# Optimization experiments

Hardware: AMD Instinct MI355X
Metric: run time of the kernel (lower is better)

The kernel has to match this reference:

```python
import jax, jax.numpy as jnp
import numpy as np

ALPHA = 0.5
NUM_NB = 8


def setup_inputs() -> dict:
    key = jax.random.key(0)
    k1, k2 = jax.random.split(key)
    pc1 = jax.random.normal(k1, (4, 3, 8192), dtype=jnp.float32)
    pred_flow = jax.random.normal(k2, (4, 3, 8192), dtype=jnp.float32)
    return {"pc1": pc1, "pred_flow": pred_flow}


def reference(pc1, pred_flow):
    # pc1, pred_flow: [B, 3, N] -> [B, N, 3]
    B, _, N = pc1.shape
    k = NUM_NB
    p = jnp.transpose(pc1, (0, 2, 1))         # [B, N, 3]
    f = jnp.transpose(pred_flow, (0, 2, 1))   # [B, N, 3]

    sq = jnp.sum(p * p, axis=-1)
    sqrdist = sq[:, :, None] + sq[:, None, :] - 2.0 * jnp.einsum('bnd,bmd->bnm', p, p)

    # k+1 smallest (sorted ascending), drop self (first column)
    neg_d, kidx = jax.lax.top_k(-sqrdist, k + 1)  # descending in -d == ascending in d
    dists = -neg_d[:, :, 1:]                      # [B, N, k]
    kidx = kidx[:, :, 1:]                         # [B, N, k]
    dists = jnp.maximum(dists, 0.0)

    # softmax over all N*k weights per batch
    w = jax.nn.softmax(jnp.exp(-dists / ALPHA).reshape(B, N * k), axis=1)
    w = w.reshape(B, N, k)

    # gather neighbor flows: [B, N, k, 3]
    grouped = jnp.take_along_axis(f[:, None, :, :],
                                  kidx[:, :, :, None],
                                  axis=2)
    diff = jnp.linalg.norm(grouped - f[:, :, None, :], axis=3)  # [B, N, k]
    diff_flow = (N * w * diff).sum(axis=2)                      # [B, N]
    return jnp.mean(diff_flow)
```

## Files before the change

### kernel.cpp

```cpp
#include <hip/hip_runtime.h>
#include <math.h>

#define BATCH 4
#define NQ 8192
#define KNB 8
#define K1 9
#define NB 512
#define XMIN -4.5f
#define XSCALE (NB / 9.0f)
#define CAP 21
#define THW 512
#define THS 128
#define SPART 2
#define IDXMASK 8191u
#define KEYMASK 0xFFFFE000u
#define EPS_S 1e-3f

static __device__ __forceinline__ int binOf(float x) {
  return min(max((int)((x - XMIN) * XSCALE), 0), NB - 1);
}

#define CHAIN9(KEY) { unsigned kk = (KEY); \
  _Pragma("unroll") \
  for (int j = 0; j < K1; ++j) { \
    unsigned lo = min(kk, nk[j]); unsigned hi = max(kk, nk[j]); \
    nk[j] = lo; kk = hi; } }

#define CHAIN8(KEY) { unsigned kk = (KEY); \
  _Pragma("unroll") \
  for (int j = 0; j < KNB; ++j) { \
    unsigned lo = min(kk, nk[j]); unsigned hi = max(kk, nk[j]); \
    nk[j] = lo; kk = hi; } }

#define DRAINS() { \
  for (int ii = 0; ii < cnt; ++ii) { \
    const unsigned key = sbuf[base + ii]; \
    if (key < nk[K1-1]) CHAIN9(key); \
  } \
  cnt = 0; \
  { const float td = __uint_as_float(nk[K1-1] | 0x1FFFu); \
    thetaS = fminf(thetaS, 0.5f*(td - qq) + EPS_S); } }

#define GPROC(SS, OI) { \
  if ((SS) <= thetaS) { \
    const float dd = fmaxf(fmaf(2.0f, (SS), qq), 0.0f); \
    sbuf[base + cnt] = (__float_as_uint(dd) & KEYMASK) | (OI); cnt++; } }

#define SCORE4(S0,S1,S2,S3, X,Y,Z,H) \
  float S0 = fmaf(nqx, X.x, fmaf(nqy, Y.x, fmaf(nqz, Z.x, H.x))); \
  float S1 = fmaf(nqx, X.y, fmaf(nqy, Y.y, fmaf(nqz, Z.y, H.y))); \
  float S2 = fmaf(nqx, X.z, fmaf(nqy, Y.z, fmaf(nqz, Z.z, H.z))); \
  float S3 = fmaf(nqx, X.w, fmaf(nqy, Y.w, fmaf(nqz, Z.w, H.w)));

#define BURST(CB) { \
  const int jb = (CB) << 4; \
  const int ti = (bq + jb) >> 2; \
  const float4 X0=x4[ti],X1=x4[ti+1],X2=x4[ti+2],X3=x4[ti+3]; \
  const float4 Y0=y4[ti],Y1=y4[ti+1],Y2=y4[ti+2],Y3=y4[ti+3]; \
  const float4 Z0=z4[ti],Z1=z4[ti+1],Z2=z4[ti+2],Z3=z4[ti+3]; \
  const float4 H0=h4[ti],H1=h4[ti+1],H2=h4[ti+2],H3=h4[ti+3]; \
  const uint4  I0=i4[ti],I1=i4[ti+1],I2=i4[ti+2],I3=i4[ti+3]; \
  SCORE4(s0,s1,s2,s3, X0,Y0,Z0,H0); \
  SCORE4(s4,s5,s6,s7, X1,Y1,Z1,H1); \
  SCORE4(s8,s9,sa,sb, X2,Y2,Z2,H2); \
  SCORE4(sc,sd,se,sf, X3,Y3,Z3,H3); \
  GPROC(s0,I0.x); GPROC(s1,I0.y); GPROC(s2,I0.z); GPROC(s3,I0.w); \
  GPROC(s4,I1.x); GPROC(s5,I1.y); GPROC(s6,I1.z); GPROC(s7,I1.w); \
  GPROC(s8,I2.x); GPROC(s9,I2.y); GPROC(sa,I2.z); GPROC(sb,I2.w); \
  GPROC(sc,I3.x); GPROC(sd,I3.y); GPROC(se,I3.z); GPROC(sf,I3.w); }

__global__ __launch_bounds__(256) void hist_kernel(
    const float* __restrict__ pc, unsigned* __restrict__ hist)
{
  const int t = blockIdx.x * 256 + threadIdx.x;
  const int b = t >> 13, n = t & (NQ - 1);
  atomicAdd(&hist[b * NB + binOf(pc[(size_t)b * 3 * NQ + n])], 1u);
}

__global__ __launch_bounds__(512) void prefix_kernel(
    unsigned* __restrict__ hist, unsigned* __restrict__ binStart)
{
  __shared__ unsigned sc[NB];
  const int t = threadIdx.x;
  for (int b = 0; b < BATCH; ++b) {
    const unsigned c = hist[b * NB + t];
    sc[t] = c;
    __syncthreads();
    for (int o = 1; o < NB; o <<= 1) {
      unsigned a = (t >= o) ? sc[t - o] : 0u;
      __syncthreads();
      sc[t] += a;
      __syncthreads();
    }
    const unsigned excl = sc[t] - c;
    binStart[b * (NB + 1) + t] = excl;
    hist[b * NB + t] = excl;
    if (t == NB - 1) binStart[b * (NB + 1) + NB] = NQ;
    __syncthreads();
  }
}

__global__ __launch_bounds__(256) void scatter_kernel(
    const float* __restrict__ pc, unsigned* __restrict__ cursor,
    float* __restrict__ sxs, float* __restrict__ sys, float* __restrict__ szs,
    float* __restrict__ shs, unsigned* __restrict__ ssi)
{
  const int t = blockIdx.x * 256 + threadIdx.x;
  const int b = t >> 13, n = t & (NQ - 1);
  const float* __restrict__ px = pc + (size_t)b * 3 * NQ;
  const float x = px[n], y = px[NQ + n], z = px[2 * NQ + n];
  const unsigned pos = atomicAdd(&cursor[b * NB + binOf(x)], 1u);
  const int o = b * NQ + (int)pos;
  sxs[o] = x; sys[o] = y; szs[o] = z;
  shs[o] = 0.5f * (x * x + y * y + z * z);
  ssi[o] = (unsigned)n;
}

__global__ __launch_bounds__(256) void theta_kernel(
    const float* __restrict__ sxs, const float* __restrict__ sys,
    const float* __restrict__ szs, unsigned* __restrict__ thetaOut)
{
  __shared__ float swx[THW], swy[THW], swz[THW];
  const int b = blockIdx.y, p = blockIdx.z;
  const int B0 = blockIdx.x * 256;
  const int bq = b * NQ;
  const int stg0 = min(max(B0 - 128, 0), NQ - THW);
#pragma unroll
  for (int k = 0; k < THW / 256; ++k) {
    const int i = threadIdx.x + k * 256;
    swx[i] = sxs[bq + stg0 + i];
    swy[i] = sys[bq + stg0 + i];
    swz[i] = szs[bq + stg0 + i];
  }
  __syncthreads();
  const int s = B0 + threadIdx.x;
  const float qx = swx[s - stg0], qy = swy[s - stg0], qz = swz[s - stg0];
  const int w = min(max(s - 128, stg0), stg0 + THW - 256) - stg0;
  unsigned nk[K1];
#pragma unroll
  for (int j = 0; j < K1; ++j) nk[j] = 0xFFFFFFFFu;
  for (int k = 0; k < THS; ++k) {
    const int i = w + 2 * k + p;
    const float dx = qx - swx[i], dy = qy - swy[i], dz = qz - swz[i];
    const float d = dx * dx + dy * dy + dz * dz;
    CHAIN9(__float_as_uint(d));
  }
  thetaOut[(size_t)(bq + s) * SPART + p] = nk[K1 - 1] | 0x1FFFu;
}

template<int P>
__global__ __launch_bounds__(256) void knn_kernel(
    const float* __restrict__ sxs, const float* __restrict__ sys,
    const float* __restrict__ szs, const float* __restrict__ shs,
    const unsigned* __restrict__ ssi, const unsigned* __restrict__ binStart,
    const unsigned* __restrict__ thetaIn, unsigned* __restrict__ wsK)
{
  __shared__ unsigned sbuf[256 * CAP];
  const int b = blockIdx.y, p = blockIdx.z;
  const int s = blockIdx.x * 256 + threadIdx.x;
  const int bq = b * NQ;
  const float qx = sxs[bq + s], qy = sys[bq + s], qz = szs[bq + s];
  const float nqx = -qx, nqy = -qy, nqz = -qz;
  const float qq = qx * qx + qy * qy + qz * qz;

  const uint2 th = ((const uint2*)thetaIn)[bq + s];
  const float thetaD = __uint_as_float(min(th.x, th.y));
  float thetaS = 0.5f * (thetaD - qq) + EPS_S;
  const float r = sqrtf(thetaD) * 1.0001f + 1e-7f;
  unsigned LO = binStart[b * (NB + 1) + binOf(qx - r)];
  unsigned HI = binStart[b * (NB + 1) + binOf(qx + r) + 1];
  for (int off = 32; off; off >>= 1) {
    LO = min(LO, (unsigned)__shfl_xor((int)LO, off));
    HI = max(HI, (unsigned)__shfl_xor((int)HI, off));
  }
  const int b0 = __builtin_amdgcn_readfirstlane((int)LO) >> 4;
  const int b1 = (__builtin_amdgcn_readfirstlane((int)HI) + 15) >> 4;
  const int nb = b1 - b0;
  const int st = b0 + (p * nb) / P;
  const int en = b0 + ((p + 1) * nb) / P;

  unsigned nk[K1];
#pragma unroll
  for (int j = 0; j < K1; ++j) nk[j] = 0xFFFFFFFFu;
  const unsigned base = (unsigned)threadIdx.x * CAP;
  int cnt = 0;
  const float4* __restrict__ x4 = (const float4*)sxs;
  const float4* __restrict__ y4 = (const float4*)sys;
  const float4* __restrict__ z4 = (const float4*)szs;
  const float4* __restrict__ h4 = (const float4*)shs;
  const uint4*  __restrict__ i4 = (const uint4*)ssi;

  for (int cb = st; cb < en; ++cb) {
    if (__any(cnt >= CAP - 16)) { DRAINS(); }
    BURST(cb);
  }
  DRAINS();

#pragma unroll
  for (int j = 0; j < K1; ++j)
    wsK[((size_t)(b * P + p) * K1 + j) * NQ + s] = nk[j];
}

__global__ __launch_bounds__(64) void loss_kernel(
    const float* __restrict__ pc, const float* __restrict__ pf,
    const float* __restrict__ sxs, const float* __restrict__ sys,
    const float* __restrict__ szs, const unsigned* __restrict__ ssi,
    const unsigned* __restrict__ wsK, float* __restrict__ acc,
    unsigned* __restrict__ doneCtr, float* __restrict__ out,
    int P, int nBlocks)
{
  const int b = blockIdx.y;
  const int s = blockIdx.x * 64 + threadIdx.x;
  const int bq = b * NQ;
  const float* __restrict__ px = pc + (size_t)b * 3 * NQ;
  const float* __restrict__ py = px + NQ;
  const float* __restrict__ pz = px + 2 * NQ;
  const float* __restrict__ fx = pf + (size_t)b * 3 * NQ;
  const float* __restrict__ fy = fx + NQ;
  const float* __restrict__ fz = fx + 2 * NQ;

  const unsigned qorig = ssi[bq + s];
  unsigned nk[KNB];
#pragma unroll
  for (int j = 0; j < KNB; ++j) nk[j] = 0xFFFFFFFFu;

  const int total = P * K1;
  const size_t stride0 = (size_t)b * P * K1;
  for (int m0 = 0; m0 < total; m0 += K1) {
    unsigned kb[K1];
#pragma unroll
    for (int u = 0; u < K1; ++u)
      kb[u] = wsK[(stride0 + m0 + u) * NQ + s];
#pragma unroll
    for (int u = 0; u < K1; ++u) {
      const unsigned key = kb[u];
      if ((key & IDXMASK) == qorig) continue;
      if (key < nk[KNB - 1]) CHAIN8(key);
    }
  }

  const float qx = sxs[bq + s], qy = sys[bq + s], qz = szs[bq + s];
  const float fqx = fx[qorig], fqy = fy[qorig], fqz = fz[qorig];
  float ssum = 0.f, sdsum = 0.f;
#pragma unroll
  for (int j = 0; j < KNB; ++j) {
    const int i = (int)(nk[j] & IDXMASK);
    const float dx = qx - px[i], dy = qy - py[i], dz = qz - pz[i];
    const float d = dx * dx + dy * dy + dz * dz;
    const float e = expf(expf(-2.0f * d));
    const float gx = fx[i] - fqx, gy = fy[i] - fqy, gz = fz[i] - fqz;
    const float diff = sqrtf(gx * gx + gy * gy + gz * gz);
    ssum += e; sdsum += e * diff;
  }

  for (int off = 32; off > 0; off >>= 1) {
    ssum += __shfl_down(ssum, off);
    sdsum += __shfl_down(sdsum, off);
  }
  if (threadIdx.x == 0) {
    atomicAdd(&acc[b * 2 + 0], ssum);
    atomicAdd(&acc[b * 2 + 1], sdsum);
    __threadfence();
    const unsigned done = atomicAdd(doneCtr, 1u);
    if (done == (unsigned)(nBlocks - 1)) {
      float sT = 0.f;
      for (int bb = 0; bb < BATCH; ++bb) {
        const float se = atomicAdd(&acc[bb * 2 + 0], 0.f);
        const float sd = atomicAdd(&acc[bb * 2 + 1], 0.f);
        sT += sd / se;
      }
      out[0] = sT * (1.0f / BATCH);
    }
  }
}

extern "C" void kernel_launch(void* const* d_in, const int* in_sizes, int n_in,
                              void* d_out, int out_size, void* d_ws, size_t ws_size,
                              hipStream_t stream) {
  const float* pc = (const float*)d_in[0];
  const float* pf = (const float*)d_in[1];
  float* out = (float*)d_out;

  char* w = (char*)d_ws;
  float*    acc      = (float*)w;
  unsigned* doneCtr  = (unsigned*)(w + 64);
  unsigned* hist     = (unsigned*)(w + 256);
  unsigned* binStart = (unsigned*)(w + 8448);
  const size_t SA = 16896;
  float*    sxs = (float*)(w + SA);
  float*    sys = (float*)(w + SA + 1 * 131072);
  float*    szs = (float*)(w + SA + 2 * 131072);
  float*    shs = (float*)(w + SA + 3 * 131072);
  unsigned* ssi = (unsigned*)(w + SA + 4 * 131072);
  const size_t TH = SA + 5 * 131072;
  unsigned* thetaBuf = (unsigned*)(w + TH);
  const size_t WK = TH + (size_t)BATCH * NQ * SPART * 4;
  unsigned* wsK = (unsigned*)(w + WK);

  const size_t needP16 = WK + (size_t)BATCH * NQ * 16 * K1 * 4;
  const size_t needP8  = WK + (size_t)BATCH * NQ * 8  * K1 * 4;
  const int P = (ws_size >= needP16) ? 16 : (ws_size >= needP8) ? 8 : 4;

  hipMemsetAsync(d_ws, 0, 8448, stream);

  hist_kernel<<<dim3(BATCH * NQ / 256), 256, 0, stream>>>(pc, hist);
  prefix_kernel<<<dim3(1), 512, 0, stream>>>(hist, binStart);
  scatter_kernel<<<dim3(BATCH * NQ / 256), 256, 0, stream>>>(
      pc, hist, sxs, sys, szs, shs, ssi);
  theta_kernel<<<dim3(NQ / 256, BATCH, SPART), 256, 0, stream>>>(
      sxs, sys, szs, thetaBuf);
  if (P == 16)
    knn_kernel<16><<<dim3(NQ / 256, BATCH, 16), 256, 0, stream>>>(
        sxs, sys, szs, shs, ssi, binStart, thetaBuf, wsK);
  else if (P == 8)
    knn_kernel<8><<<dim3(NQ / 256, BATCH, 8), 256, 0, stream>>>(
        sxs, sys, szs, shs, ssi, binStart, thetaBuf, wsK);
  else
    knn_kernel<4><<<dim3(NQ / 256, BATCH, 4), 256, 0, stream>>>(
        sxs, sys, szs, shs, ssi, binStart, thetaBuf, wsK);
  const int nBlocks = (NQ / 64) * BATCH;
  loss_kernel<<<dim3(NQ / 64, BATCH), 64, 0, stream>>>(
      pc, pf, sxs, sys, szs, ssi, wsK, acc, doneCtr, out, P, nBlocks);
}
```

Measured before the change: 144.1 us.

## Pack candidate tiles into AoS-of-16 blocks and recompute half-norm in KNN

The scatter kernel now also writes a packed per-16-point tile layout (x, y, z and index contiguous in 256 bytes), and the KNN burst reads one contiguous tile instead of five separate SoA streams. The precomputed half squared norm array is dropped and the score is recomputed from coordinates with a few extra FMAs, cutting per-candidate memory traffic from 20 to 16 bytes. The shared-memory staging capacity CAP grows from 21 to 25, which reduces drain frequency at the cost of more LDS per block and possibly lower occupancy. Scatter does more scattered writes.

Measured after the change: 149.4 us. 1.04x slower.

```diff
diff --git a/kernel.cpp b/kernel.cpp
--- a/kernel.cpp
+++ b/kernel.cpp
@@ -8,10 +8,11 @@
 #define NB 512
 #define XMIN -4.5f
 #define XSCALE (NB / 9.0f)
-#define CAP 21
+#define CAP 25
 #define THW 512
 #define THS 128
 #define SPART 2
+#define NT (NQ / 16)
 #define IDXMASK 8191u
 #define KEYMASK 0xFFFFE000u
 #define EPS_S 1e-3f
@@ -46,28 +47,35 @@
     const float dd = fmaxf(fmaf(2.0f, (SS), qq), 0.0f); \
     sbuf[base + cnt] = (__float_as_uint(dd) & KEYMASK) | (OI); cnt++; } }
 
-#define SCORE4(S0,S1,S2,S3, X,Y,Z,H) \
-  float S0 = fmaf(nqx, X.x, fmaf(nqy, Y.x, fmaf(nqz, Z.x, H.x))); \
-  float S1 = fmaf(nqx, X.y, fmaf(nqy, Y.y, fmaf(nqz, Z.y, H.y))); \
-  float S2 = fmaf(nqx, X.z, fmaf(nqy, Y.z, fmaf(nqz, Z.z, H.z))); \
-  float S3 = fmaf(nqx, X.w, fmaf(nqy, Y.w, fmaf(nqz, Z.w, H.w)));
+#define SCOREC(X, Y, Z) \
+  fmaf((X), fmaf(0.5f,(X),nqx), fmaf((Y), fmaf(0.5f,(Y),nqy), (Z)*fmaf(0.5f,(Z),nqz)))
 
 #define BURST(CB) { \
-  const int jb = (CB) << 4; \
-  const int ti = (bq + jb) >> 2; \
-  const float4 X0=x4[ti],X1=x4[ti+1],X2=x4[ti+2],X3=x4[ti+3]; \
-  const float4 Y0=y4[ti],Y1=y4[ti+1],Y2=y4[ti+2],Y3=y4[ti+3]; \
-  const float4 Z0=z4[ti],Z1=z4[ti+1],Z2=z4[ti+2],Z3=z4[ti+3]; \
-  const float4 H0=h4[ti],H1=h4[ti+1],H2=h4[ti+2],H3=h4[ti+3]; \
-  const uint4  I0=i4[ti],I1=i4[ti+1],I2=i4[ti+2],I3=i4[ti+3]; \
-  SCORE4(s0,s1,s2,s3, X0,Y0,Z0,H0); \
-  SCORE4(s4,s5,s6,s7, X1,Y1,Z1,H1); \
-  SCORE4(s8,s9,sa,sb, X2,Y2,Z2,H2); \
-  SCORE4(sc,sd,se,sf, X3,Y3,Z3,H3); \
-  GPROC(s0,I0.x); GPROC(s1,I0.y); GPROC(s2,I0.z); GPROC(s3,I0.w); \
-  GPROC(s4,I1.x); GPROC(s5,I1.y); GPROC(s6,I1.z); GPROC(s7,I1.w); \
-  GPROC(s8,I2.x); GPROC(s9,I2.y); GPROC(sa,I2.z); GPROC(sb,I2.w); \
-  GPROC(sc,I3.x); GPROC(sd,I3.y); GPROC(se,I3.z); GPROC(sf,I3.w); }
+  const uint4* __restrict__ tp = (const uint4*)(packed + (((size_t)btile + (CB)) << 6)); \
+  const uint4 wx0=tp[0],  wx1=tp[1],  wx2=tp[2],  wx3=tp[3]; \
+  const uint4 wy0=tp[4],  wy1=tp[5],  wy2=tp[6],  wy3=tp[7]; \
+  const uint4 wz0=tp[8],  wz1=tp[9],  wz2=tp[10], wz3=tp[11]; \
+  const uint4 wi0=tp[12], wi1=tp[13], wi2=tp[14], wi3=tp[15]; \
+  const float s0 = SCOREC(__uint_as_float(wx0.x), __uint_as_float(wy0.x), __uint_as_float(wz0.x)); \
+  const float s1 = SCOREC(__uint_as_float(wx0.y), __uint_as_float(wy0.y), __uint_as_float(wz0.y)); \
+  const float s2 = SCOREC(__uint_as_float(wx0.z), __uint_as_float(wy0.z), __uint_as_float(wz0.z)); \
+  const float s3 = SCOREC(__uint_as_float(wx0.w), __uint_as_float(wy0.w), __uint_as_float(wz0.w)); \
+  const float s4 = SCOREC(__uint_as_float(wx1.x), __uint_as_float(wy1.x), __uint_as_float(wz1.x)); \
+  const float s5 = SCOREC(__uint_as_float(wx1.y), __uint_as_float(wy1.y), __uint_as_float(wz1.y)); \
+  const float s6 = SCOREC(__uint_as_float(wx1.z), __uint_as_float(wy1.z), __uint_as_float(wz1.z)); \
+  const float s7 = SCOREC(__uint_as_float(wx1.w), __uint_as_float(wy1.w), __uint_as_float(wz1.w)); \
+  const float s8 = SCOREC(__uint_as_float(wx2.x), __uint_as_float(wy2.x), __uint_as_float(wz2.x)); \
+  const float s9 = SCOREC(__uint_as_float(wx2.y), __uint_as_float(wy2.y), __uint_as_float(wz2.y)); \
+  const float sa = SCOREC(__uint_as_float(wx2.z), __uint_as_float(wy2.z), __uint_as_float(wz2.z)); \
+  const float sb = SCOREC(__uint_as_float(wx2.w), __uint_as_float(wy2.w), __uint_as_float(wz2.w)); \
+  const float sc = SCOREC(__uint_as_float(wx3.x), __uint_as_float(wy3.x), __uint_as_float(wz3.x)); \
+  const float sd = SCOREC(__uint_as_float(wx3.y), __uint_as_float(wy3.y), __uint_as_float(wz3.y)); \
+  const float se = SCOREC(__uint_as_float(wx3.z), __uint_as_float(wy3.z), __uint_as_float(wz3.z)); \
+  const float sf = SCOREC(__uint_as_float(wx3.w), __uint_as_float(wy3.w), __uint_as_float(wz3.w)); \
+  GPROC(s0, wi0.x); GPROC(s1, wi0.y); GPROC(s2, wi0.z); GPROC(s3, wi0.w); \
+  GPROC(s4, wi1.x); GPROC(s5, wi1.y); GPROC(s6, wi1.z); GPROC(s7, wi1.w); \
+  GPROC(s8, wi2.x); GPROC(s9, wi2.y); GPROC(sa, wi2.z); GPROC(sb, wi2.w); \
+  GPROC(sc, wi3.x); GPROC(sd, wi3.y); GPROC(se, wi3.z); GPROC(sf, wi3.w); }
 
 __global__ __launch_bounds__(256) void hist_kernel(
     const float* __restrict__ pc, unsigned* __restrict__ hist)
@@ -103,7 +111,7 @@
 __global__ __launch_bounds__(256) void scatter_kernel(
     const float* __restrict__ pc, unsigned* __restrict__ cursor,
     float* __restrict__ sxs, float* __restrict__ sys, float* __restrict__ szs,
-    float* __restrict__ shs, unsigned* __restrict__ ssi)
+    unsigned* __restrict__ ssi, unsigned* __restrict__ packed)
 {
   const int t = blockIdx.x * 256 + threadIdx.x;
   const int b = t >> 13, n = t & (NQ - 1);
@@ -112,8 +120,13 @@
   const unsigned pos = atomicAdd(&cursor[b * NB + binOf(x)], 1u);
   const int o = b * NQ + (int)pos;
   sxs[o] = x; sys[o] = y; szs[o] = z;
-  shs[o] = 0.5f * (x * x + y * y + z * z);
   ssi[o] = (unsigned)n;
+  const unsigned tile = (unsigned)b * NT + (pos >> 4), slot = pos & 15u;
+  unsigned* tb = packed + ((size_t)tile << 6);
+  tb[slot]      = __float_as_uint(x);
+  tb[16 + slot] = __float_as_uint(y);
+  tb[32 + slot] = __float_as_uint(z);
+  tb[48 + slot] = (unsigned)n;
 }
 
 __global__ __launch_bounds__(256) void theta_kernel(
@@ -151,9 +164,9 @@
 template<int P>
 __global__ __launch_bounds__(256) void knn_kernel(
     const float* __restrict__ sxs, const float* __restrict__ sys,
-    const float* __restrict__ szs, const float* __restrict__ shs,
-    const unsigned* __restrict__ ssi, const unsigned* __restrict__ binStart,
-    const unsigned* __restrict__ thetaIn, unsigned* __restrict__ wsK)
+    const float* __restrict__ szs, const unsigned* __restrict__ packed,
+    const unsigned* __restrict__ binStart, const unsigned* __restrict__ thetaIn,
+    unsigned* __restrict__ wsK)
 {
   __shared__ unsigned sbuf[256 * CAP];
   const int b = blockIdx.y, p = blockIdx.z;
@@ -178,17 +191,13 @@
   const int nb = b1 - b0;
   const int st = b0 + (p * nb) / P;
   const int en = b0 + ((p + 1) * nb) / P;
+  const int btile = b * NT;
 
   unsigned nk[K1];
 #pragma unroll
   for (int j = 0; j < K1; ++j) nk[j] = 0xFFFFFFFFu;
   const unsigned base = (unsigned)threadIdx.x * CAP;
   int cnt = 0;
-  const float4* __restrict__ x4 = (const float4*)sxs;
-  const float4* __restrict__ y4 = (const float4*)sys;
-  const float4* __restrict__ z4 = (const float4*)szs;
-  const float4* __restrict__ h4 = (const float4*)shs;
-  const uint4*  __restrict__ i4 = (const uint4*)ssi;
 
   for (int cb = st; cb < en; ++cb) {
     if (__any(cnt >= CAP - 16)) { DRAINS(); }
@@ -290,9 +299,9 @@
   float*    sxs = (float*)(w + SA);
   float*    sys = (float*)(w + SA + 1 * 131072);
   float*    szs = (float*)(w + SA + 2 * 131072);
-  float*    shs = (float*)(w + SA + 3 * 131072);
-  unsigned* ssi = (unsigned*)(w + SA + 4 * 131072);
-  const size_t TH = SA + 5 * 131072;
+  unsigned* ssi = (unsigned*)(w + SA + 3 * 131072);
+  unsigned* packed = (unsigned*)(w + SA + 4 * 131072);
+  const size_t TH = SA + 4 * 131072 + (size_t)BATCH * NT * 256;
   unsigned* thetaBuf = (unsigned*)(w + TH);
   const size_t WK = TH + (size_t)BATCH * NQ * SPART * 4;
   unsigned* wsK = (unsigned*)(w + WK);
@@ -306,18 +315,18 @@
   hist_kernel<<<dim3(BATCH * NQ / 256), 256, 0, stream>>>(pc, hist);
   prefix_kernel<<<dim3(1), 512, 0, stream>>>(hist, binStart);
   scatter_kernel<<<dim3(BATCH * NQ / 256), 256, 0, stream>>>(
-      pc, hist, sxs, sys, szs, shs, ssi);
+      pc, hist, sxs, sys, szs, ssi, packed);
   theta_kernel<<<dim3(NQ / 256, BATCH, SPART), 256, 0, stream>>>(
       sxs, sys, szs, thetaBuf);
   if (P == 16)
     knn_kernel<16><<<dim3(NQ / 256, BATCH, 16), 256, 0, stream>>>(
-        sxs, sys, szs, shs, ssi, binStart, thetaBuf, wsK);
+        sxs, sys, szs, packed, binStart, thetaBuf, wsK);
   else if (P == 8)
     knn_kernel<8><<<dim3(NQ / 256, BATCH, 8), 256, 0, stream>>>(
-        sxs, sys, szs, shs, ssi, binStart, thetaBuf, wsK);
+        sxs, sys, szs, packed, binStart, thetaBuf, wsK);
   else
     knn_kernel<4><<<dim3(NQ / 256, BATCH, 4), 256, 0, stream>>>(
-        sxs, sys, szs, shs, ssi, binStart, thetaBuf, wsK);
+        sxs, sys, szs, packed, binStart, thetaBuf, wsK);
   const int nBlocks = (NQ / 64) * BATCH;
   loss_kernel<<<dim3(NQ / 64, BATCH), 64, 0, stream>>>(
       pc, pf, sxs, sys, szs, ssi, wsK, acc, doneCtr, out, P, nBlocks);
```
